# Optimization experiments

Measured on AMD Instinct MI355X. Metric: run time of the kernel, lower is better.

The kernel has to match this reference:

```python
import jax, jax.numpy as jnp
import numpy as np

B = 32768      # rows
L = 512        # sequence_length
H = 1024       # inter_layer_size
E = 128        # encoding_size
K = 8          # number of (shifting_type, transformer_ID) combinations / decoders


def setup_inputs() -> dict:
    key = jax.random.key(0)
    ks = jax.random.split(key, 8)
    feats = jax.random.normal(ks[0], (B, L), jnp.float32)
    ids = jax.random.randint(ks[1], (B,), 0, K).astype(jnp.float32)
    x = jnp.concatenate([feats, ids[:, None]], axis=1)  # [B, L+1], last col = combination ID

    def init_w(k, shape, fan_in):
        return jax.random.normal(k, shape, jnp.float32) / np.float32(np.sqrt(fan_in))

    # shared encoder: Linear(L->H), Linear(H->E)  (weights stored [in, out])
    We1 = init_w(ks[2], (L, H), L); be1 = jnp.zeros((H,), jnp.float32)
    We2 = init_w(ks[3], (H, E), H); be2 = jnp.zeros((E,), jnp.float32)
    # per-ID decoders stacked along expert dim K: Linear(E->H), Linear(H->L)
    Wd1 = init_w(ks[4], (K, E, H), E); bd1 = jnp.zeros((K, H), jnp.float32)
    Wd2 = init_w(ks[5], (K, H, L), H); bd2 = jnp.zeros((K, L), jnp.float32)
    return dict(x=x, We1=We1, be1=be1, We2=We2, be2=be2,
                Wd1=Wd1, bd1=bd1, Wd2=Wd2, bd2=bd2)


def reference(x, We1, be1, We2, be2, Wd1, bd1, Wd2, bd2):
    seq_len = We1.shape[0]
    n_experts = Wd1.shape[0]
    ids = x[:, seq_len].astype(jnp.int32)          # routing column
    # torch code emits rows grouped by unique ID (torch.unique returns sorted ids);
    # jnp.argsort is stable, so within-group original order is preserved.
    order = jnp.argsort(ids)
    xs = x[order, :seq_len]                        # [B, L] grouped features
    ids_s = ids[order]                             # [B]

    # shared encoder MLP (LeakyReLU slope 0.01, torch default)
    h = jax.nn.leaky_relu(xs @ We1 + be1)          # [B, H]
    z = jax.nn.leaky_relu(h @ We2 + be2)           # [B, E]

    # dense expert dispatch: run every decoder, select per-row expert via one-hot
    hd = jax.nn.leaky_relu(jnp.einsum('be,keh->kbh', z, Wd1) + bd1[:, None, :])  # [K, B, H]
    y_all = jnp.einsum('kbh,khl->kbl', hd, Wd2) + bd2[:, None, :]                # [K, B, L]
    onehot = (ids_s[None, :] == jnp.arange(n_experts)[:, None]).astype(y_all.dtype)  # [K, B]
    return jnp.einsum('kb,kbl->bl', onehot, y_all)  # [B, L]
```

## Files before the change

kernel.cpp:

```cpp
#include <hip/hip_runtime.h>
#include <hip/hip_bf16.h>

#define B_ROWS 32768
#define L_DIM 512
#define H_DIM 1024
#define E_DIM 128
#define K_EXP 8
#define NBLK 128
#define MAXT 264
#define MAXB (MAXT * 128)

typedef __bf16 bf16x8 __attribute__((ext_vector_type(8)));
typedef float f32x4 __attribute__((ext_vector_type(4)));

__device__ __forceinline__ void gload16(const void* src, void* dst) {
    __builtin_amdgcn_global_load_lds(
        (const __attribute__((address_space(1))) unsigned int*)src,
        (__attribute__((address_space(3))) unsigned int*)dst, 16, 0, 0);
}

#define M_NT 0
#define M_SEG 1
#define M_SEGP 10
#define M_CNT 19
#define M_TEXP 27

__global__ void k_ids_hist(const float* __restrict__ x, int* __restrict__ ids,
                           int* __restrict__ hist) {
    __shared__ int lh[K_EXP];
    int t = threadIdx.x;
    if (t < K_EXP) lh[t] = 0;
    __syncthreads();
    int i = blockIdx.x * 256 + t;
    int id = (int)x[(size_t)i * (L_DIM + 1) + L_DIM];
    ids[i] = id;
    atomicAdd(&lh[id], 1);
    __syncthreads();
    if (t < K_EXP) hist[blockIdx.x * K_EXP + t] = lh[t];
}

__global__ void k_scan(const int* __restrict__ hist, int* __restrict__ base,
                       int* __restrict__ meta, int* __restrict__ order_pad) {
    __shared__ int c[K_EXP];
    __shared__ int sp[K_EXP + 1];
    __shared__ int scnt[K_EXP];
    int k = threadIdx.x;
    if (k < K_EXP) {
        int run = 0;
        for (int b = 0; b < NBLK; ++b) {
            base[b * K_EXP + k] = run;
            run += hist[b * K_EXP + k];
        }
        c[k] = run;
    }
    __syncthreads();
    if (k == 0) {
        int s = 0, p = 0;
        for (int e = 0; e < K_EXP; ++e) {
            meta[M_SEG + e] = s;
            meta[M_SEGP + e] = p;
            meta[M_CNT + e] = c[e];
            sp[e] = p;
            scnt[e] = c[e];
            s += c[e];
            p += ((c[e] + 127) >> 7) << 7;
        }
        meta[M_SEG + K_EXP] = s;
        meta[M_SEGP + K_EXP] = p;
        sp[K_EXP] = p;
        int nT = p >> 7;
        meta[M_NT] = nT;
        for (int e = 0; e < K_EXP; ++e)
            for (int t2 = sp[e] >> 7; t2 < sp[e + 1] >> 7; ++t2)
                meta[M_TEXP + t2] = e;
        for (int t2 = nT; t2 < MAXT; ++t2) meta[M_TEXP + t2] = 0;
    }
    __syncthreads();
    if (k < K_EXP) {
        int s0 = sp[k];
        for (int b = 0; b < NBLK; ++b) base[b * K_EXP + k] += s0;
    }
    for (int e = 0; e < K_EXP; ++e) {
        int st = sp[e] + scnt[e], en = sp[e + 1];
        for (int p2 = st + k; p2 < en; p2 += 64) order_pad[p2] = 0;
    }
    for (int p2 = sp[K_EXP] + k; p2 < MAXB; p2 += 64) order_pad[p2] = 0;
}

__global__ void k_order(const int* __restrict__ ids, const int* __restrict__ base,
                        int* __restrict__ order) {
    __shared__ int sid[256];
    int t = threadIdx.x;
    int i = blockIdx.x * 256 + t;
    int my = ids[i];
    sid[t] = my;
    __syncthreads();
    int rank = 0;
    for (int j = 0; j < t; ++j) rank += (sid[j] == my) ? 1 : 0;
    order[base[blockIdx.x * K_EXP + my] + rank] = i;
}

__global__ void k_gather(const float* __restrict__ x, const int* __restrict__ order,
                         __hip_bfloat16* __restrict__ xs) {
    int idx = blockIdx.x * 256 + threadIdx.x;
    int p = idx >> 7;
    int c4 = (idx & 127) << 2;
    int src = order[p];
    const float* sp = x + (size_t)src * (L_DIM + 1) + c4;
    __hip_bfloat16 v[4];
    v[0] = __float2bfloat16(sp[0]);
    v[1] = __float2bfloat16(sp[1]);
    v[2] = __float2bfloat16(sp[2]);
    v[3] = __float2bfloat16(sp[3]);
    *(uint2*)(xs + (size_t)p * L_DIM + c4) = *(uint2*)v;
}

__global__ void k_transpose(const float* __restrict__ W, __hip_bfloat16* __restrict__ Wt,
                            int KDim, int NDim) {
    __shared__ float tile[32][33];
    int k0 = blockIdx.x << 5, n0 = blockIdx.y << 5;
    const float* Wb = W + (size_t)blockIdx.z * KDim * NDim;
    __hip_bfloat16* Wtb = Wt + (size_t)blockIdx.z * KDim * NDim;
    int tx = threadIdx.x & 31, ty = threadIdx.x >> 5;
    for (int i = ty; i < 32; i += 8)
        tile[i][tx] = Wb[(size_t)(k0 + i) * NDim + n0 + tx];
    __syncthreads();
    for (int i = ty; i < 32; i += 8)
        Wtb[(size_t)(n0 + i) * KDim + k0 + tx] = __float2bfloat16(tile[tx][i]);
}

template <int KD, int ND, bool GROUPED, bool LEAKY, bool OUT_BF16, bool MAPROW>
__launch_bounds__(256, 2)
__global__ void gemm_w(const __hip_bfloat16* __restrict__ A,
                       const __hip_bfloat16* __restrict__ Bt,
                       const float* __restrict__ bias,
                       void* __restrict__ Cout,
                       const int* __restrict__ meta) {
    constexpr int NNT = ND / 256;
    constexpr int TOT = MAXT * NNT;
    static_assert(TOT % 8 == 0, "XCD chunking needs TOT % 8 == 0");
    constexpr int ASZ = 128 * 32;
    constexpr int SLOT = ASZ + 256 * 32;
    constexpr int NK = KD / 32;

    __shared__ __align__(16) __hip_bfloat16 smem[3 * SLOT];
    const int id = blockIdx.x;
    const int wg = (id & 7) * (TOT / 8) + (id >> 3);
    const int mt = wg / NNT, nt = wg % NNT;
    const int m0 = mt << 7, n0 = nt << 8;
    const __hip_bfloat16* Bp = Bt;
    const float* bp = bias;
    int e = 0;
    if (GROUPED) {
        e = meta[M_TEXP + mt];
        Bp += (size_t)e * KD * ND;
        bp += (size_t)e * ND;
    }
    const int t = threadIdx.x, w = t >> 6, l = t & 63;
    const int g = l >> 4, li = l & 15;
    const int r0 = l >> 2, s0 = l & 3;

    f32x4 acc[8][4];
#pragma unroll
    for (int i = 0; i < 8; ++i)
#pragma unroll
        for (int j = 0; j < 4; ++j) acc[i][j] = (f32x4){0.f, 0.f, 0.f, 0.f};

    auto stage = [&](int b, int kt) {
#pragma unroll
        for (int qi = 0; qi < 2; ++qi) {
            int q = 2 * w + qi;
            int r = q * 16 + r0;
            int ksg = s0 ^ ((r >> 1) & 3);
            gload16(A + (size_t)(m0 + r) * KD + kt * 32 + ksg * 8,
                    &smem[b * SLOT + q * 512]);
        }
#pragma unroll
        for (int qi = 0; qi < 4; ++qi) {
            int q = 4 * w + qi;
            int r = q * 16 + r0;
            int ksg = s0 ^ ((r >> 1) & 3);
            gload16(Bp + (size_t)(n0 + r) * KD + kt * 32 + ksg * 8,
                    &smem[b * SLOT + ASZ + q * 512]);
        }
    };

    stage(0, 0);
    stage(1, 1);
    int b = 0;
    for (int kt = 0; kt < NK; ++kt) {
        if (kt == NK - 1)
            asm volatile("s_waitcnt vmcnt(0)\ns_barrier" ::: "memory");
        else
            asm volatile("s_waitcnt vmcnt(6)\ns_barrier" ::: "memory");
        __builtin_amdgcn_sched_barrier(0);
        if (kt + 2 < NK) stage((b + 2 >= 3) ? b - 1 : b + 2, kt + 2);
        bf16x8 af[8], bfr[4];
#pragma unroll
        for (int fm = 0; fm < 8; ++fm) {
            int rr = fm * 16 + li;
            int ss = g ^ ((rr >> 1) & 3);
            af[fm] = *(const bf16x8*)&smem[b * SLOT + rr * 32 + ss * 8];
        }
#pragma unroll
        for (int fn = 0; fn < 4; ++fn) {
            int cc = w * 64 + fn * 16 + li;
            int ss = g ^ ((cc >> 1) & 3);
            bfr[fn] = *(const bf16x8*)&smem[b * SLOT + ASZ + cc * 32 + ss * 8];
        }
        __builtin_amdgcn_s_setprio(1);
#pragma unroll
        for (int fm = 0; fm < 8; ++fm)
#pragma unroll
            for (int fn = 0; fn < 4; ++fn)
                acc[fm][fn] = __builtin_amdgcn_mfma_f32_16x16x32_bf16(
                    af[fm], bfr[fn], acc[fm][fn], 0, 0, 0);
        __builtin_amdgcn_s_setprio(0);
        b = (b + 1 >= 3) ? 0 : b + 1;
    }

    float bv[4];
#pragma unroll
    for (int fn = 0; fn < 4; ++fn) bv[fn] = bp[n0 + w * 64 + fn * 16 + li];
    int se = 0, sp2 = 0, ce = 0;
    if (MAPROW) { se = meta[M_SEG + e]; sp2 = meta[M_SEGP + e]; ce = meta[M_CNT + e]; }
#pragma unroll
    for (int fm = 0; fm < 8; ++fm)
#pragma unroll
        for (int i = 0; i < 4; ++i) {
            int rp = m0 + fm * 16 + g * 4 + i;
#pragma unroll
            for (int fn = 0; fn < 4; ++fn) {
                float v = acc[fm][fn][i] + bv[fn];
                if (LEAKY) v = v > 0.f ? v : 0.01f * v;
                int col = n0 + w * 64 + fn * 16 + li;
                if (MAPROW) {
                    int local = rp - sp2;
                    if (local < ce)
                        ((float*)Cout)[(size_t)(se + local) * ND + col] = v;
                } else if (OUT_BF16) {
                    ((__hip_bfloat16*)Cout)[(size_t)rp * ND + col] = __float2bfloat16(v);
                } else {
                    ((float*)Cout)[(size_t)rp * ND + col] = v;
                }
            }
        }
}

template <int KD, int ND, bool LEAKY>
__launch_bounds__(256)
__global__ void gemm_u64(const __hip_bfloat16* __restrict__ A,
                         const __hip_bfloat16* __restrict__ Bt,
                         const float* __restrict__ bias,
                         __hip_bfloat16* __restrict__ Cout) {
    constexpr int BM = 64;
    constexpr int NNT = ND / 128;
    constexpr int NMT = MAXB / BM;
    constexpr int TOT = NMT * NNT;
    static_assert(TOT % 8 == 0, "XCD chunking needs TOT % 8 == 0");
    constexpr int ACH = BM * 32;
    constexpr int SLOT = ACH + 128 * 32;
    constexpr int NK = KD / 32;

    __shared__ __align__(16) __hip_bfloat16 smem[3 * SLOT];
    const int id = blockIdx.x;
    const int wg = (id & 7) * (TOT / 8) + (id >> 3);
    const int mt = wg / NNT, nt = wg % NNT;
    const int n0 = nt << 7;
    const int m0 = mt * BM;
    const int t = threadIdx.x, w = t >> 6, l = t & 63;
    const int wm = w >> 1, wn = w & 1, g = l >> 4, li = l & 15;
    const int r0 = l >> 2, s0 = l & 3;

    f32x4 acc[2][4];
#pragma unroll
    for (int i = 0; i < 2; ++i)
#pragma unroll
        for (int j = 0; j < 4; ++j) acc[i][j] = (f32x4){0.f, 0.f, 0.f, 0.f};

    auto stage = [&](int b, int kt) {
        {
            int q = w, r = q * 16 + r0;
            int ksg = s0 ^ ((r >> 1) & 3);
            gload16(A + (size_t)(m0 + r) * KD + kt * 32 + ksg * 8,
                    &smem[b * SLOT + q * 512]);
        }
#pragma unroll
        for (int qi = 0; qi < 2; ++qi) {
            int q = 2 * w + qi, r = q * 16 + r0;
            int ksg = s0 ^ ((r >> 1) & 3);
            gload16(Bt + (size_t)(n0 + r) * KD + kt * 32 + ksg * 8,
                    &smem[b * SLOT + ACH + q * 512]);
        }
    };

    stage(0, 0);
    stage(1, 1);
    int b = 0;
    for (int kt = 0; kt < NK; ++kt) {
        if (kt == NK - 1)
            asm volatile("s_waitcnt vmcnt(0)\ns_barrier" ::: "memory");
        else
            asm volatile("s_waitcnt vmcnt(3)\ns_barrier" ::: "memory");
        __builtin_amdgcn_sched_barrier(0);
        if (kt + 2 < NK) stage((b + 2 >= 3) ? b - 1 : b + 2, kt + 2);
        bf16x8 af[2], bfr[4];
#pragma unroll
        for (int fm = 0; fm < 2; ++fm) {
            int rr = wm * 32 + fm * 16 + li;
            int ss = g ^ ((rr >> 1) & 3);
            af[fm] = *(const bf16x8*)&smem[b * SLOT + rr * 32 + ss * 8];
        }
#pragma unroll
        for (int fn = 0; fn < 4; ++fn) {
            int cc = wn * 64 + fn * 16 + li;
            int ss = g ^ ((cc >> 1) & 3);
            bfr[fn] = *(const bf16x8*)&smem[b * SLOT + ACH + cc * 32 + ss * 8];
        }
        __builtin_amdgcn_s_setprio(1);
#pragma unroll
        for (int fm = 0; fm < 2; ++fm)
#pragma unroll
            for (int fn = 0; fn < 4; ++fn)
                acc[fm][fn] = __builtin_amdgcn_mfma_f32_16x16x32_bf16(
                    af[fm], bfr[fn], acc[fm][fn], 0, 0, 0);
        __builtin_amdgcn_s_setprio(0);
        b = (b + 1 >= 3) ? 0 : b + 1;
    }

    float bv[4];
#pragma unroll
    for (int fn = 0; fn < 4; ++fn) bv[fn] = bias[n0 + wn * 64 + fn * 16 + li];
#pragma unroll
    for (int fm = 0; fm < 2; ++fm)
#pragma unroll
        for (int i = 0; i < 4; ++i) {
            int r = m0 + wm * 32 + fm * 16 + g * 4 + i;
#pragma unroll
            for (int fn = 0; fn < 4; ++fn) {
                float v = acc[fm][fn][i] + bv[fn];
                if (LEAKY) v = v > 0.f ? v : 0.01f * v;
                Cout[(size_t)r * ND + n0 + wn * 64 + fn * 16 + li] = __float2bfloat16(v);
            }
        }
}

extern "C" void kernel_launch(void* const* d_in, const int* in_sizes, int n_in,
                              void* d_out, int out_size, void* d_ws, size_t ws_size,
                              hipStream_t stream) {
    (void)in_sizes; (void)n_in; (void)out_size; (void)ws_size;
    const float* x   = (const float*)d_in[0];
    const float* We1 = (const float*)d_in[1];
    const float* be1 = (const float*)d_in[2];
    const float* We2 = (const float*)d_in[3];
    const float* be2 = (const float*)d_in[4];
    const float* Wd1 = (const float*)d_in[5];
    const float* bd1 = (const float*)d_in[6];
    const float* Wd2 = (const float*)d_in[7];
    const float* bd2 = (const float*)d_in[8];
    float* out = (float*)d_out;

    char* w = (char*)d_ws;
    auto alloc = [&](size_t bytes) {
        char* p = w;
        w += (bytes + 255) & ~(size_t)255;
        return p;
    };
    int* ids       = (int*)alloc((size_t)B_ROWS * 4);
    int* order_pad = (int*)alloc((size_t)MAXB * 4);
    int* hist      = (int*)alloc((size_t)NBLK * K_EXP * 4);
    int* base      = (int*)alloc((size_t)NBLK * K_EXP * 4);
    int* meta      = (int*)alloc((size_t)(M_TEXP + MAXT) * 4);
    __hip_bfloat16* xs   = (__hip_bfloat16*)alloc((size_t)MAXB * L_DIM * 2);
    __hip_bfloat16* hbuf = (__hip_bfloat16*)alloc((size_t)MAXB * H_DIM * 2);
    __hip_bfloat16* zbuf = (__hip_bfloat16*)alloc((size_t)MAXB * E_DIM * 2);
    __hip_bfloat16* Wt1  = (__hip_bfloat16*)alloc((size_t)L_DIM * H_DIM * 2);
    __hip_bfloat16* Wt2  = (__hip_bfloat16*)alloc((size_t)H_DIM * E_DIM * 2);
    __hip_bfloat16* Wd1t = (__hip_bfloat16*)alloc((size_t)K_EXP * E_DIM * H_DIM * 2);
    __hip_bfloat16* Wd2t = (__hip_bfloat16*)alloc((size_t)K_EXP * H_DIM * L_DIM * 2);

    k_ids_hist<<<NBLK, 256, 0, stream>>>(x, ids, hist);
    k_scan<<<1, 64, 0, stream>>>(hist, base, meta, order_pad);
    k_order<<<NBLK, 256, 0, stream>>>(ids, base, order_pad);
    k_gather<<<(MAXB * (L_DIM / 4)) / 256, 256, 0, stream>>>(x, order_pad, xs);

    k_transpose<<<dim3(L_DIM / 32, H_DIM / 32, 1), 256, 0, stream>>>(We1, Wt1, L_DIM, H_DIM);
    k_transpose<<<dim3(H_DIM / 32, E_DIM / 32, 1), 256, 0, stream>>>(We2, Wt2, H_DIM, E_DIM);
    k_transpose<<<dim3(E_DIM / 32, H_DIM / 32, K_EXP), 256, 0, stream>>>(Wd1, Wd1t, E_DIM, H_DIM);
    k_transpose<<<dim3(H_DIM / 32, L_DIM / 32, K_EXP), 256, 0, stream>>>(Wd2, Wd2t, H_DIM, L_DIM);

    gemm_w<L_DIM, H_DIM, false, true, true, false>
        <<<MAXT * (H_DIM / 256), 256, 0, stream>>>(xs, Wt1, be1, hbuf, meta);
    gemm_u64<H_DIM, E_DIM, true>
        <<<(MAXB / 64) * (E_DIM / 128), 256, 0, stream>>>(hbuf, Wt2, be2, zbuf);
    gemm_w<E_DIM, H_DIM, true, true, true, false>
        <<<MAXT * (H_DIM / 256), 256, 0, stream>>>(zbuf, Wd1t, bd1, hbuf, meta);
    gemm_w<H_DIM, L_DIM, true, false, false, true>
        <<<MAXT * (L_DIM / 256), 256, 0, stream>>>(hbuf, Wd2t, bd2, out, meta);
}
```

Before: 229.8 us.

## Use 256x256 eight-wave GEMM tiles with 64-wide K ping-pong and regroup padding

Expert segments are now padded to 256 rows, and the large GEMMs (encoder layer 1 and decoder layer 2) use a new 512-thread kernel with 256x256 tiles. It double-buffers 64-wide K tiles with an XOR swizzle and interleaves LDS reads, MFMA bursts and half-tile async stages behind barriers. Decoder layer 1 (K=128) gets a dedicated 128x128 kernel that looks up its expert per 256-row group. The goal is more data reuse per LDS byte and better overlap of loads with MFMA, at the cost of more padding rows, more barriers and heavier register pressure.

```diff
diff --git a/kernel.cpp b/kernel.cpp
--- a/kernel.cpp
+++ b/kernel.cpp
@@ -7,8 +7,8 @@
 #define E_DIM 128
 #define K_EXP 8
 #define NBLK 128
-#define MAXT 264
-#define MAXB (MAXT * 128)
+#define MAXT2 136
+#define MAXB2 (MAXT2 * 256)
 
 typedef __bf16 bf16x8 __attribute__((ext_vector_type(8)));
 typedef float f32x4 __attribute__((ext_vector_type(4)));
@@ -63,17 +63,17 @@
             sp[e] = p;
             scnt[e] = c[e];
             s += c[e];
-            p += ((c[e] + 127) >> 7) << 7;
+            p += ((c[e] + 255) >> 8) << 8;
         }
         meta[M_SEG + K_EXP] = s;
         meta[M_SEGP + K_EXP] = p;
         sp[K_EXP] = p;
-        int nT = p >> 7;
+        int nT = p >> 8;
         meta[M_NT] = nT;
         for (int e = 0; e < K_EXP; ++e)
-            for (int t2 = sp[e] >> 7; t2 < sp[e + 1] >> 7; ++t2)
+            for (int t2 = sp[e] >> 8; t2 < (sp[e + 1] >> 8); ++t2)
                 meta[M_TEXP + t2] = e;
-        for (int t2 = nT; t2 < MAXT; ++t2) meta[M_TEXP + t2] = 0;
+        for (int t2 = nT; t2 < MAXT2; ++t2) meta[M_TEXP + t2] = 0;
     }
     __syncthreads();
     if (k < K_EXP) {
@@ -84,7 +84,7 @@
         int st = sp[e] + scnt[e], en = sp[e + 1];
         for (int p2 = st + k; p2 < en; p2 += 64) order_pad[p2] = 0;
     }
-    for (int p2 = sp[K_EXP] + k; p2 < MAXB; p2 += 64) order_pad[p2] = 0;
+    for (int p2 = sp[K_EXP] + k; p2 < MAXB2; p2 += 64) order_pad[p2] = 0;
 }
 
 __global__ void k_order(const int* __restrict__ ids, const int* __restrict__ base,
@@ -129,25 +129,32 @@
         Wtb[(size_t)(n0 + i) * KDim + k0 + tx] = __float2bfloat16(tile[tx][i]);
 }
 
+#define BARRIER asm volatile("s_barrier" ::: "memory")
+#define LGKM0   asm volatile("s_waitcnt lgkmcnt(0)" ::: "memory")
+#define VM4BAR  asm volatile("s_waitcnt vmcnt(4)\ns_barrier" ::: "memory")
+#define VM0BAR  asm volatile("s_waitcnt vmcnt(0)\ns_barrier" ::: "memory")
+
 template <int KD, int ND, bool GROUPED, bool LEAKY, bool OUT_BF16, bool MAPROW>
-__launch_bounds__(256, 2)
-__global__ void gemm_w(const __hip_bfloat16* __restrict__ A,
-                       const __hip_bfloat16* __restrict__ Bt,
-                       const float* __restrict__ bias,
-                       void* __restrict__ Cout,
-                       const int* __restrict__ meta) {
+__launch_bounds__(512, 2)
+__global__ void gemm8(const __hip_bfloat16* __restrict__ A,
+                      const __hip_bfloat16* __restrict__ Bt,
+                      const float* __restrict__ bias,
+                      void* __restrict__ Cout,
+                      const int* __restrict__ meta) {
     constexpr int NNT = ND / 256;
-    constexpr int TOT = MAXT * NNT;
-    static_assert(TOT % 8 == 0, "XCD chunking needs TOT % 8 == 0");
-    constexpr int ASZ = 128 * 32;
-    constexpr int SLOT = ASZ + 256 * 32;
-    constexpr int NK = KD / 32;
-
-    __shared__ __align__(16) __hip_bfloat16 smem[3 * SLOT];
+    constexpr int TOT = MAXT2 * NNT;
+    static_assert(TOT % 8 == 0, "XCD chunking");
+    constexpr int NKT = KD / 64;
+    constexpr int NI = NKT / 2;
+    static_assert(NKT % 2 == 0, "even K-tiles");
+    constexpr int DBUF = 32768;
+
+    __shared__ __align__(16) __hip_bfloat16 smem[2 * DBUF];
+
     const int id = blockIdx.x;
     const int wg = (id & 7) * (TOT / 8) + (id >> 3);
     const int mt = wg / NNT, nt = wg % NNT;
-    const int m0 = mt << 7, n0 = nt << 8;
+    const int m0 = mt << 8, n0 = nt << 8;
     const __hip_bfloat16* Bp = Bt;
     const float* bp = bias;
     int e = 0;
@@ -156,9 +163,11 @@
         Bp += (size_t)e * KD * ND;
         bp += (size_t)e * ND;
     }
-    const int t = threadIdx.x, w = t >> 6, l = t & 63;
+    const int t = threadIdx.x;
+    const int w = t >> 6, l = t & 63;
+    const int wm = w >> 2, wn = w & 3;
     const int g = l >> 4, li = l & 15;
-    const int r0 = l >> 2, s0 = l & 3;
+    const int sr = l >> 3, sc = l & 7;
 
     f32x4 acc[8][4];
 #pragma unroll
@@ -166,74 +175,89 @@
 #pragma unroll
         for (int j = 0; j < 4; ++j) acc[i][j] = (f32x4){0.f, 0.f, 0.f, 0.f};
 
-    auto stage = [&](int b, int kt) {
-#pragma unroll
-        for (int qi = 0; qi < 2; ++qi) {
-            int q = 2 * w + qi;
-            int r = q * 16 + r0;
-            int ksg = s0 ^ ((r >> 1) & 3);
-            gload16(A + (size_t)(m0 + r) * KD + kt * 32 + ksg * 8,
-                    &smem[b * SLOT + q * 512]);
-        }
-#pragma unroll
-        for (int qi = 0; qi < 4; ++qi) {
-            int q = 4 * w + qi;
-            int r = q * 16 + r0;
-            int ksg = s0 ^ ((r >> 1) & 3);
-            gload16(Bp + (size_t)(n0 + r) * KD + kt * 32 + ksg * 8,
-                    &smem[b * SLOT + ASZ + q * 512]);
-        }
-    };
-
-    stage(0, 0);
-    stage(1, 1);
-    int b = 0;
-    for (int kt = 0; kt < NK; ++kt) {
-        if (kt == NK - 1)
-            asm volatile("s_waitcnt vmcnt(0)\ns_barrier" ::: "memory");
-        else
-            asm volatile("s_waitcnt vmcnt(6)\ns_barrier" ::: "memory");
+    auto stageH = [&](int d, int which, int half, int kt) {
+        const __hip_bfloat16* src = which ? Bp : A;
+        const int rb = (which ? n0 : m0) + half * 128;
+#pragma unroll
+        for (int q = 0; q < 2; ++q) {
+            int rl = (q * 8 + w) * 8;
+            gload16(src + (size_t)(rb + rl + sr) * KD + (size_t)(kt * 8 + (sc ^ sr)) * 8,
+                    &smem[d * DBUF + which * 16384 + half * 8192 + rl * 64]);
+        }
+    };
+
+    bf16x8 a0[8], a1[8], bb[2];
+    auto LDA = [&](int d, int ksub, bf16x8* ar) {
+#pragma unroll
+        for (int fm = 0; fm < 8; ++fm) {
+            int r = wm * 128 + fm * 16 + li;
+            ar[fm] = *(const bf16x8*)&smem[d * DBUF + r * 64 + (((ksub << 2) + g) ^ (r & 7)) * 8];
+        }
+    };
+    auto LDB = [&](int d, int np, int ksub) {
+#pragma unroll
+        for (int j = 0; j < 2; ++j) {
+            int r = wn * 64 + (np * 2 + j) * 16 + li;
+            bb[j] = *(const bf16x8*)&smem[d * DBUF + 16384 + r * 64 + (((ksub << 2) + g) ^ (r & 7)) * 8];
+        }
+    };
+    auto MM = [&](int np, bf16x8* ar) {
+        __builtin_amdgcn_s_setprio(1);
+#pragma unroll
+        for (int fm = 0; fm < 8; ++fm) {
+            acc[fm][np * 2 + 0] = __builtin_amdgcn_mfma_f32_16x16x32_bf16(
+                ar[fm], bb[0], acc[fm][np * 2 + 0], 0, 0, 0);
+            acc[fm][np * 2 + 1] = __builtin_amdgcn_mfma_f32_16x16x32_bf16(
+                ar[fm], bb[1], acc[fm][np * 2 + 1], 0, 0, 0);
+        }
+        __builtin_amdgcn_s_setprio(0);
+    };
+
+    stageH(0, 0, 0, 0); stageH(0, 0, 1, 0);
+    stageH(0, 1, 0, 0); stageH(0, 1, 1, 0);
+    stageH(1, 0, 0, 1); stageH(1, 0, 1, 1);
+    VM4BAR;
+    __builtin_amdgcn_sched_barrier(0);
+
+    for (int i = 0; i < NI; ++i) {
+        const int E2 = 2 * i + 2, O1 = 2 * i + 1, O2 = 2 * i + 3;
+        const bool more = (i + 1 < NI);
+        LDA(0, 0, a0); LDB(0, 0, 0); stageH(1, 1, 0, O1);
+        BARRIER; LGKM0; MM(0, a0); BARRIER;
+        LDA(0, 1, a1); LDB(0, 0, 1); stageH(1, 1, 1, O1);
+        BARRIER; LGKM0; MM(0, a1); BARRIER;
+        LDB(0, 1, 0); if (more) stageH(0, 0, 0, E2);
+        BARRIER; LGKM0; MM(1, a0); BARRIER;
+        LDB(0, 1, 1); if (more) stageH(0, 0, 1, E2);
+        BARRIER; LGKM0; MM(1, a1);
+        if (more) { VM4BAR; } else { VM0BAR; }
         __builtin_amdgcn_sched_barrier(0);
-        if (kt + 2 < NK) stage((b + 2 >= 3) ? b - 1 : b + 2, kt + 2);
-        bf16x8 af[8], bfr[4];
-#pragma unroll
-        for (int fm = 0; fm < 8; ++fm) {
-            int rr = fm * 16 + li;
-            int ss = g ^ ((rr >> 1) & 3);
-            af[fm] = *(const bf16x8*)&smem[b * SLOT + rr * 32 + ss * 8];
-        }
-#pragma unroll
-        for (int fn = 0; fn < 4; ++fn) {
-            int cc = w * 64 + fn * 16 + li;
-            int ss = g ^ ((cc >> 1) & 3);
-            bfr[fn] = *(const bf16x8*)&smem[b * SLOT + ASZ + cc * 32 + ss * 8];
-        }
-        __builtin_amdgcn_s_setprio(1);
-#pragma unroll
-        for (int fm = 0; fm < 8; ++fm)
-#pragma unroll
-            for (int fn = 0; fn < 4; ++fn)
-                acc[fm][fn] = __builtin_amdgcn_mfma_f32_16x16x32_bf16(
-                    af[fm], bfr[fn], acc[fm][fn], 0, 0, 0);
-        __builtin_amdgcn_s_setprio(0);
-        b = (b + 1 >= 3) ? 0 : b + 1;
+        LDA(1, 0, a0); LDB(1, 0, 0); if (more) stageH(0, 1, 0, E2);
+        BARRIER; LGKM0; MM(0, a0); BARRIER;
+        LDA(1, 1, a1); LDB(1, 0, 1); if (more) stageH(0, 1, 1, E2);
+        BARRIER; LGKM0; MM(0, a1); BARRIER;
+        LDB(1, 1, 0); if (more) stageH(1, 0, 0, O2);
+        BARRIER; LGKM0; MM(1, a0); BARRIER;
+        LDB(1, 1, 1); if (more) stageH(1, 0, 1, O2);
+        BARRIER; LGKM0; MM(1, a1);
+        if (more) { VM4BAR; __builtin_amdgcn_sched_barrier(0); }
     }
 
     float bv[4];
 #pragma unroll
-    for (int fn = 0; fn < 4; ++fn) bv[fn] = bp[n0 + w * 64 + fn * 16 + li];
+    for (int fn = 0; fn < 4; ++fn) bv[fn] = bp[n0 + wn * 64 + fn * 16 + li];
     int se = 0, sp2 = 0, ce = 0;
     if (MAPROW) { se = meta[M_SEG + e]; sp2 = meta[M_SEGP + e]; ce = meta[M_CNT + e]; }
 #pragma unroll
     for (int fm = 0; fm < 8; ++fm)
 #pragma unroll
-        for (int i = 0; i < 4; ++i) {
-            int rp = m0 + fm * 16 + g * 4 + i;
+        for (int ii = 0; ii < 4; ++ii) {
+            int rp = m0 + wm * 128 + fm * 16 + g * 4 + ii;
 #pragma unroll
             for (int fn = 0; fn < 4; ++fn) {
-                float v = acc[fm][fn][i] + bv[fn];
+                float v = acc[fm][fn][ii] + bv[fn];
                 if (LEAKY) v = v > 0.f ? v : 0.01f * v;
-                int col = n0 + w * 64 + fn * 16 + li;
+                int col = n0 + wn * 64 + fn * 16 + li;
                 if (MAPROW) {
                     int local = rp - sp2;
                     if (local < ce)
@@ -247,6 +271,102 @@
         }
 }
 
+template <int ND, bool LEAKY>
+__launch_bounds__(256)
+__global__ void gemm_g3(const __hip_bfloat16* __restrict__ A,
+                        const __hip_bfloat16* __restrict__ Bt,
+                        const float* __restrict__ bias,
+                        __hip_bfloat16* __restrict__ Cout,
+                        const int* __restrict__ meta) {
+    constexpr int KD = 128;
+    constexpr int NNT = ND / 128;
+    constexpr int TOT = (MAXB2 / 128) * NNT;
+    static_assert(TOT % 8 == 0, "XCD chunking");
+    constexpr int SLOT = 2 * 128 * 32;
+    constexpr int NK = KD / 32;
+    __shared__ __align__(16) __hip_bfloat16 smem[3 * SLOT];
+    const int id = blockIdx.x;
+    const int wg = (id & 7) * (TOT / 8) + (id >> 3);
+    const int mt = wg / NNT, nt = wg % NNT;
+    const int e = meta[M_TEXP + (mt >> 1)];
+    const int m0 = mt << 7, n0 = nt << 7;
+    const __hip_bfloat16* Bp = Bt + (size_t)e * KD * ND;
+    const float* bp = bias + (size_t)e * ND;
+    const int t = threadIdx.x, w = t >> 6, l = t & 63;
+    const int wm = w >> 1, wn = w & 1, g = l >> 4, li = l & 15;
+    const int q0 = 2 * w, r0 = l >> 2, s0 = l & 3;
+
+    f32x4 acc[4][4];
+#pragma unroll
+    for (int i = 0; i < 4; ++i)
+#pragma unroll
+        for (int j = 0; j < 4; ++j) acc[i][j] = (f32x4){0.f, 0.f, 0.f, 0.f};
+
+    auto stage = [&](int b, int kt) {
+#pragma unroll
+        for (int qi = 0; qi < 2; ++qi) {
+            int q = q0 + qi, r = q * 16 + r0;
+            int ksg = s0 ^ ((r >> 1) & 3);
+            gload16(A + (size_t)(m0 + r) * KD + kt * 32 + ksg * 8,
+                    &smem[b * SLOT + q * 512]);
+        }
+#pragma unroll
+        for (int qi = 0; qi < 2; ++qi) {
+            int q = q0 + qi, r = q * 16 + r0;
+            int ksg = s0 ^ ((r >> 1) & 3);
+            gload16(Bp + (size_t)(n0 + r) * KD + kt * 32 + ksg * 8,
+                    &smem[b * SLOT + 4096 + q * 512]);
+        }
+    };
+
+    stage(0, 0);
+    stage(1, 1);
+    int b = 0;
+    for (int kt = 0; kt < NK; ++kt) {
+        if (kt == NK - 1) { VM0BAR; } else { VM4BAR; }
+        __builtin_amdgcn_sched_barrier(0);
+        if (kt + 2 < NK) stage((b + 2 >= 3) ? b - 1 : b + 2, kt + 2);
+        bf16x8 af[4], bfr[4];
+#pragma unroll
+        for (int fm = 0; fm < 4; ++fm) {
+            int rr = wm * 64 + fm * 16 + li;
+            int ss = g ^ ((rr >> 1) & 3);
+            af[fm] = *(const bf16x8*)&smem[b * SLOT + rr * 32 + ss * 8];
+        }
+#pragma unroll
+        for (int fn = 0; fn < 4; ++fn) {
+            int cc = wn * 64 + fn * 16 + li;
+            int ss = g ^ ((cc >> 1) & 3);
+            bfr[fn] = *(const bf16x8*)&smem[b * SLOT + 4096 + cc * 32 + ss * 8];
+        }
+        __builtin_amdgcn_s_setprio(1);
+#pragma unroll
+        for (int fm = 0; fm < 4; ++fm)
+#pragma unroll
+            for (int fn = 0; fn < 4; ++fn)
+                acc[fm][fn] = __builtin_amdgcn_mfma_f32_16x16x32_bf16(
+                    af[fm], bfr[fn], acc[fm][fn], 0, 0, 0);
+        __builtin_amdgcn_s_setprio(0);
+        b = (b + 1 >= 3) ? 0 : b + 1;
+    }
+
+    float bv[4];
+#pragma unroll
+    for (int fn = 0; fn < 4; ++fn) bv[fn] = bp[n0 + wn * 64 + fn * 16 + li];
+#pragma unroll
+    for (int fm = 0; fm < 4; ++fm)
+#pragma unroll
+        for (int i = 0; i < 4; ++i) {
+            int r = m0 + wm * 64 + fm * 16 + g * 4 + i;
+#pragma unroll
+            for (int fn = 0; fn < 4; ++fn) {
+                float v = acc[fm][fn][i] + bv[fn];
+                if (LEAKY) v = v > 0.f ? v : 0.01f * v;
+                Cout[(size_t)r * ND + n0 + wn * 64 + fn * 16 + li] = __float2bfloat16(v);
+            }
+        }
+}
+
 template <int KD, int ND, bool LEAKY>
 __launch_bounds__(256)
 __global__ void gemm_u64(const __hip_bfloat16* __restrict__ A,
@@ -255,9 +375,9 @@
                          __hip_bfloat16* __restrict__ Cout) {
     constexpr int BM = 64;
     constexpr int NNT = ND / 128;
-    constexpr int NMT = MAXB / BM;
+    constexpr int NMT = MAXB2 / BM;
     constexpr int TOT = NMT * NNT;
-    static_assert(TOT % 8 == 0, "XCD chunking needs TOT % 8 == 0");
+    static_assert(TOT % 8 == 0, "XCD chunking");
     constexpr int ACH = BM * 32;
     constexpr int SLOT = ACH + 128 * 32;
     constexpr int NK = KD / 32;
@@ -367,13 +487,13 @@
         return p;
     };
     int* ids       = (int*)alloc((size_t)B_ROWS * 4);
-    int* order_pad = (int*)alloc((size_t)MAXB * 4);
+    int* order_pad = (int*)alloc((size_t)MAXB2 * 4);
     int* hist      = (int*)alloc((size_t)NBLK * K_EXP * 4);
     int* base      = (int*)alloc((size_t)NBLK * K_EXP * 4);
-    int* meta      = (int*)alloc((size_t)(M_TEXP + MAXT) * 4);
-    __hip_bfloat16* xs   = (__hip_bfloat16*)alloc((size_t)MAXB * L_DIM * 2);
-    __hip_bfloat16* hbuf = (__hip_bfloat16*)alloc((size_t)MAXB * H_DIM * 2);
-    __hip_bfloat16* zbuf = (__hip_bfloat16*)alloc((size_t)MAXB * E_DIM * 2);
+    int* meta      = (int*)alloc((size_t)(M_TEXP + MAXT2) * 4);
+    __hip_bfloat16* xs   = (__hip_bfloat16*)alloc((size_t)MAXB2 * L_DIM * 2);
+    __hip_bfloat16* hbuf = (__hip_bfloat16*)alloc((size_t)MAXB2 * H_DIM * 2);
+    __hip_bfloat16* zbuf = (__hip_bfloat16*)alloc((size_t)MAXB2 * E_DIM * 2);
     __hip_bfloat16* Wt1  = (__hip_bfloat16*)alloc((size_t)L_DIM * H_DIM * 2);
     __hip_bfloat16* Wt2  = (__hip_bfloat16*)alloc((size_t)H_DIM * E_DIM * 2);
     __hip_bfloat16* Wd1t = (__hip_bfloat16*)alloc((size_t)K_EXP * E_DIM * H_DIM * 2);
@@ -382,19 +502,19 @@
     k_ids_hist<<<NBLK, 256, 0, stream>>>(x, ids, hist);
     k_scan<<<1, 64, 0, stream>>>(hist, base, meta, order_pad);
     k_order<<<NBLK, 256, 0, stream>>>(ids, base, order_pad);
-    k_gather<<<(MAXB * (L_DIM / 4)) / 256, 256, 0, stream>>>(x, order_pad, xs);
+    k_gather<<<(MAXB2 * (L_DIM / 4)) / 256, 256, 0, stream>>>(x, order_pad, xs);
 
     k_transpose<<<dim3(L_DIM / 32, H_DIM / 32, 1), 256, 0, stream>>>(We1, Wt1, L_DIM, H_DIM);
     k_transpose<<<dim3(H_DIM / 32, E_DIM / 32, 1), 256, 0, stream>>>(We2, Wt2, H_DIM, E_DIM);
     k_transpose<<<dim3(E_DIM / 32, H_DIM / 32, K_EXP), 256, 0, stream>>>(Wd1, Wd1t, E_DIM, H_DIM);
     k_transpose<<<dim3(H_DIM / 32, L_DIM / 32, K_EXP), 256, 0, stream>>>(Wd2, Wd2t, H_DIM, L_DIM);
 
-    gemm_w<L_DIM, H_DIM, false, true, true, false>
-        <<<MAXT * (H_DIM / 256), 256, 0, stream>>>(xs, Wt1, be1, hbuf, meta);
+    gemm8<L_DIM, H_DIM, false, true, true, false>
+        <<<MAXT2 * (H_DIM / 256), 512, 0, stream>>>(xs, Wt1, be1, hbuf, meta);
     gemm_u64<H_DIM, E_DIM, true>
-        <<<(MAXB / 64) * (E_DIM / 128), 256, 0, stream>>>(hbuf, Wt2, be2, zbuf);
-    gemm_w<E_DIM, H_DIM, true, true, true, false>
-        <<<MAXT * (H_DIM / 256), 256, 0, stream>>>(zbuf, Wd1t, bd1, hbuf, meta);
-    gemm_w<H_DIM, L_DIM, true, false, false, true>
-        <<<MAXT * (L_DIM / 256), 256, 0, stream>>>(hbuf, Wd2t, bd2, out, meta);
-}
+        <<<(MAXB2 / 64) * (E_DIM / 128), 256, 0, stream>>>(hbuf, Wt2, be2, zbuf);
+    gemm_g3<H_DIM, true>
+        <<<(MAXB2 / 128) * (H_DIM / 128), 256, 0, stream>>>(zbuf, Wd1t, bd1, hbuf, meta);
+    gemm8<H_DIM, L_DIM, true, false, false, true>
+        <<<MAXT2 * (L_DIM / 256), 512, 0, stream>>>(hbuf, Wd2t, bd2, out, meta);
+}
```

New measurement: 286.0 us. +24.4%, slower.

## Fuse encoder-out and decoder-in GEMMs via LDS, merge transposes, retile GEMMs

Applied to the files above, without the earlier changes.

The second encoder GEMM (H->E) and the first decoder GEMM (E->H) now run in one kernel per 64-row tile. The latent z stays in swizzled LDS instead of making a round trip through a global buffer. The four weight-transpose launches become one kernel that dispatches on block index. The first and last GEMMs move from 128x256 tiles with 8x4 fragments per wave to 128x128 tiles with a 2x2 wave grid. This trades more blocks and less register pressure for more reloading of the A tiles. The fused kernel writes its output over the hidden buffer it reads, which relies on each block reading only its own rows.

```diff
diff --git a/kernel.cpp b/kernel.cpp
--- a/kernel.cpp
+++ b/kernel.cpp
@@ -115,73 +115,80 @@
     *(uint2*)(xs + (size_t)p * L_DIM + c4) = *(uint2*)v;
 }
 
-__global__ void k_transpose(const float* __restrict__ W, __hip_bfloat16* __restrict__ Wt,
-                            int KDim, int NDim) {
+__global__ void k_wtrans(const float* __restrict__ We1, const float* __restrict__ We2,
+                         const float* __restrict__ Wd1, const float* __restrict__ Wd2,
+                         __hip_bfloat16* __restrict__ Wt1, __hip_bfloat16* __restrict__ Wt2,
+                         __hip_bfloat16* __restrict__ Wd1t, __hip_bfloat16* __restrict__ Wd2t) {
     __shared__ float tile[32][33];
-    int k0 = blockIdx.x << 5, n0 = blockIdx.y << 5;
-    const float* Wb = W + (size_t)blockIdx.z * KDim * NDim;
-    __hip_bfloat16* Wtb = Wt + (size_t)blockIdx.z * KDim * NDim;
+    int b = blockIdx.x;
+    const float* W;
+    __hip_bfloat16* Wt;
+    int KDim, NDim, local;
+    if (b < 512)       { W = We1; Wt = Wt1; KDim = 512;  NDim = 1024; local = b; }
+    else if (b < 640)  { W = We2; Wt = Wt2; KDim = 1024; NDim = 128;  local = b - 512; }
+    else if (b < 1664) {
+        int lb = b - 640;
+        int e = lb >> 7;
+        local = lb & 127;
+        KDim = 128; NDim = 1024;
+        W = Wd1 + (size_t)e * KDim * NDim;
+        Wt = Wd1t + (size_t)e * KDim * NDim;
+    } else {
+        int lb = b - 1664;
+        int e = lb >> 9;
+        local = lb & 511;
+        KDim = 1024; NDim = 512;
+        W = Wd2 + (size_t)e * KDim * NDim;
+        Wt = Wd2t + (size_t)e * KDim * NDim;
+    }
+    int ntK = KDim >> 5;
+    int k0 = (local % ntK) << 5, n0 = (local / ntK) << 5;
     int tx = threadIdx.x & 31, ty = threadIdx.x >> 5;
     for (int i = ty; i < 32; i += 8)
-        tile[i][tx] = Wb[(size_t)(k0 + i) * NDim + n0 + tx];
+        tile[i][tx] = W[(size_t)(k0 + i) * NDim + n0 + tx];
     __syncthreads();
     for (int i = ty; i < 32; i += 8)
-        Wtb[(size_t)(n0 + i) * KDim + k0 + tx] = __float2bfloat16(tile[tx][i]);
-}
-
-template <int KD, int ND, bool GROUPED, bool LEAKY, bool OUT_BF16, bool MAPROW>
-__launch_bounds__(256, 2)
-__global__ void gemm_w(const __hip_bfloat16* __restrict__ A,
-                       const __hip_bfloat16* __restrict__ Bt,
-                       const float* __restrict__ bias,
-                       void* __restrict__ Cout,
-                       const int* __restrict__ meta) {
-    constexpr int NNT = ND / 256;
+        Wt[(size_t)(n0 + i) * KDim + k0 + tx] = __float2bfloat16(tile[tx][i]);
+}
+
+__global__ __launch_bounds__(256) void gemm_g1(const __hip_bfloat16* __restrict__ A,
+                                               const __hip_bfloat16* __restrict__ Bt,
+                                               const float* __restrict__ bias,
+                                               __hip_bfloat16* __restrict__ Cout) {
+    constexpr int KD = L_DIM, ND = H_DIM;
+    constexpr int NNT = ND / 128;
     constexpr int TOT = MAXT * NNT;
-    static_assert(TOT % 8 == 0, "XCD chunking needs TOT % 8 == 0");
-    constexpr int ASZ = 128 * 32;
-    constexpr int SLOT = ASZ + 256 * 32;
+    constexpr int SLOT = 2 * 128 * 32;
     constexpr int NK = KD / 32;
-
     __shared__ __align__(16) __hip_bfloat16 smem[3 * SLOT];
     const int id = blockIdx.x;
     const int wg = (id & 7) * (TOT / 8) + (id >> 3);
     const int mt = wg / NNT, nt = wg % NNT;
-    const int m0 = mt << 7, n0 = nt << 8;
-    const __hip_bfloat16* Bp = Bt;
-    const float* bp = bias;
-    int e = 0;
-    if (GROUPED) {
-        e = meta[M_TEXP + mt];
-        Bp += (size_t)e * KD * ND;
-        bp += (size_t)e * ND;
-    }
+    const int m0 = mt << 7, n0 = nt << 7;
     const int t = threadIdx.x, w = t >> 6, l = t & 63;
-    const int g = l >> 4, li = l & 15;
-    const int r0 = l >> 2, s0 = l & 3;
-
-    f32x4 acc[8][4];
-#pragma unroll
-    for (int i = 0; i < 8; ++i)
+    const int wm = w >> 1, wn = w & 1, g = l >> 4, li = l & 15;
+    const int q0 = 2 * w, r0 = l >> 2, s0 = l & 3;
+
+    f32x4 acc[4][4];
+#pragma unroll
+    for (int i = 0; i < 4; ++i)
 #pragma unroll
         for (int j = 0; j < 4; ++j) acc[i][j] = (f32x4){0.f, 0.f, 0.f, 0.f};
 
     auto stage = [&](int b, int kt) {
 #pragma unroll
         for (int qi = 0; qi < 2; ++qi) {
-            int q = 2 * w + qi;
-            int r = q * 16 + r0;
+            int q = q0 + qi, r = q * 16 + r0;
             int ksg = s0 ^ ((r >> 1) & 3);
             gload16(A + (size_t)(m0 + r) * KD + kt * 32 + ksg * 8,
                     &smem[b * SLOT + q * 512]);
         }
 #pragma unroll
-        for (int qi = 0; qi < 4; ++qi) {
-            int q = 4 * w + qi;
-            int r = q * 16 + r0;
-            int ksg = s0 ^ ((r >> 1) & 3);
-            gload16(Bp + (size_t)(n0 + r) * KD + kt * 32 + ksg * 8,
-                    &smem[b * SLOT + ASZ + q * 512]);
+        for (int qi = 0; qi < 2; ++qi) {
+            int q = q0 + qi, r = q * 16 + r0;
+            int ksg = s0 ^ ((r >> 1) & 3);
+            gload16(Bt + (size_t)(n0 + r) * KD + kt * 32 + ksg * 8,
+                    &smem[b * SLOT + 4096 + q * 512]);
         }
     };
 
@@ -192,25 +199,25 @@
         if (kt == NK - 1)
             asm volatile("s_waitcnt vmcnt(0)\ns_barrier" ::: "memory");
         else
-            asm volatile("s_waitcnt vmcnt(6)\ns_barrier" ::: "memory");
+            asm volatile("s_waitcnt vmcnt(4)\ns_barrier" ::: "memory");
         __builtin_amdgcn_sched_barrier(0);
         if (kt + 2 < NK) stage((b + 2 >= 3) ? b - 1 : b + 2, kt + 2);
-        bf16x8 af[8], bfr[4];
-#pragma unroll
-        for (int fm = 0; fm < 8; ++fm) {
-            int rr = fm * 16 + li;
+        bf16x8 af[4], bfr[4];
+#pragma unroll
+        for (int fm = 0; fm < 4; ++fm) {
+            int rr = wm * 64 + fm * 16 + li;
             int ss = g ^ ((rr >> 1) & 3);
             af[fm] = *(const bf16x8*)&smem[b * SLOT + rr * 32 + ss * 8];
         }
 #pragma unroll
         for (int fn = 0; fn < 4; ++fn) {
-            int cc = w * 64 + fn * 16 + li;
+            int cc = wn * 64 + fn * 16 + li;
             int ss = g ^ ((cc >> 1) & 3);
-            bfr[fn] = *(const bf16x8*)&smem[b * SLOT + ASZ + cc * 32 + ss * 8];
+            bfr[fn] = *(const bf16x8*)&smem[b * SLOT + 4096 + cc * 32 + ss * 8];
         }
         __builtin_amdgcn_s_setprio(1);
 #pragma unroll
-        for (int fm = 0; fm < 8; ++fm)
+        for (int fm = 0; fm < 4; ++fm)
 #pragma unroll
             for (int fn = 0; fn < 4; ++fn)
                 acc[fm][fn] = __builtin_amdgcn_mfma_f32_16x16x32_bf16(
@@ -221,76 +228,230 @@
 
     float bv[4];
 #pragma unroll
-    for (int fn = 0; fn < 4; ++fn) bv[fn] = bp[n0 + w * 64 + fn * 16 + li];
-    int se = 0, sp2 = 0, ce = 0;
-    if (MAPROW) { se = meta[M_SEG + e]; sp2 = meta[M_SEGP + e]; ce = meta[M_CNT + e]; }
-#pragma unroll
-    for (int fm = 0; fm < 8; ++fm)
+    for (int fn = 0; fn < 4; ++fn) bv[fn] = bias[n0 + wn * 64 + fn * 16 + li];
+#pragma unroll
+    for (int fm = 0; fm < 4; ++fm)
 #pragma unroll
         for (int i = 0; i < 4; ++i) {
-            int rp = m0 + fm * 16 + g * 4 + i;
+            int r = m0 + wm * 64 + fm * 16 + g * 4 + i;
 #pragma unroll
             for (int fn = 0; fn < 4; ++fn) {
                 float v = acc[fm][fn][i] + bv[fn];
-                if (LEAKY) v = v > 0.f ? v : 0.01f * v;
-                int col = n0 + w * 64 + fn * 16 + li;
-                if (MAPROW) {
-                    int local = rp - sp2;
-                    if (local < ce)
-                        ((float*)Cout)[(size_t)(se + local) * ND + col] = v;
-                } else if (OUT_BF16) {
-                    ((__hip_bfloat16*)Cout)[(size_t)rp * ND + col] = __float2bfloat16(v);
-                } else {
-                    ((float*)Cout)[(size_t)rp * ND + col] = v;
+                v = v > 0.f ? v : 0.01f * v;
+                Cout[(size_t)r * ND + n0 + wn * 64 + fn * 16 + li] = __float2bfloat16(v);
+            }
+        }
+}
+
+__global__ __launch_bounds__(256) void gemm_g23(const __hip_bfloat16* __restrict__ h,
+                                                const __hip_bfloat16* __restrict__ Wt2,
+                                                const float* __restrict__ be2,
+                                                const __hip_bfloat16* __restrict__ Wd1t,
+                                                const float* __restrict__ bd1,
+                                                __hip_bfloat16* __restrict__ hd,
+                                                const int* __restrict__ meta) {
+    constexpr int SLOTA = 64 * 32 + 128 * 32;
+    constexpr int SLOTB = 128 * 32;
+    constexpr int NKA = H_DIM / 32;
+    __shared__ __align__(16) __hip_bfloat16 smem[3 * SLOTA + 64 * 128];
+    __hip_bfloat16* zl = smem + 3 * SLOTA;
+
+    const int id = blockIdx.x;
+    const int wg = (id & 7) * 66 + (id >> 3);
+    const int m0 = wg << 6;
+    const int e = meta[M_TEXP + (wg >> 1)];
+    const int t = threadIdx.x, w = t >> 6, l = t & 63;
+    const int wm = w >> 1, wn = w & 1, g = l >> 4, li = l & 15;
+    const int r0 = l >> 2, s0 = l & 3;
+
+    f32x4 accA[2][4];
+#pragma unroll
+    for (int i = 0; i < 2; ++i)
+#pragma unroll
+        for (int j = 0; j < 4; ++j) accA[i][j] = (f32x4){0.f, 0.f, 0.f, 0.f};
+
+    auto stageA = [&](int b, int kt) {
+        {
+            int q = w, r = q * 16 + r0;
+            int ksg = s0 ^ ((r >> 1) & 3);
+            gload16(h + (size_t)(m0 + r) * H_DIM + kt * 32 + ksg * 8,
+                    &smem[b * SLOTA + q * 512]);
+        }
+#pragma unroll
+        for (int qi = 0; qi < 2; ++qi) {
+            int q = 2 * w + qi, r = q * 16 + r0;
+            int ksg = s0 ^ ((r >> 1) & 3);
+            gload16(Wt2 + (size_t)r * H_DIM + kt * 32 + ksg * 8,
+                    &smem[b * SLOTA + 2048 + q * 512]);
+        }
+    };
+
+    stageA(0, 0);
+    stageA(1, 1);
+    int b = 0;
+    for (int kt = 0; kt < NKA; ++kt) {
+        if (kt == NKA - 1)
+            asm volatile("s_waitcnt vmcnt(0)\ns_barrier" ::: "memory");
+        else
+            asm volatile("s_waitcnt vmcnt(3)\ns_barrier" ::: "memory");
+        __builtin_amdgcn_sched_barrier(0);
+        if (kt + 2 < NKA) stageA((b + 2 >= 3) ? b - 1 : b + 2, kt + 2);
+        bf16x8 af[2], bfr[4];
+#pragma unroll
+        for (int fm = 0; fm < 2; ++fm) {
+            int rr = wm * 32 + fm * 16 + li;
+            int ss = g ^ ((rr >> 1) & 3);
+            af[fm] = *(const bf16x8*)&smem[b * SLOTA + rr * 32 + ss * 8];
+        }
+#pragma unroll
+        for (int fn = 0; fn < 4; ++fn) {
+            int cc = wn * 64 + fn * 16 + li;
+            int ss = g ^ ((cc >> 1) & 3);
+            bfr[fn] = *(const bf16x8*)&smem[b * SLOTA + 2048 + cc * 32 + ss * 8];
+        }
+        __builtin_amdgcn_s_setprio(1);
+#pragma unroll
+        for (int fm = 0; fm < 2; ++fm)
+#pragma unroll
+            for (int fn = 0; fn < 4; ++fn)
+                accA[fm][fn] = __builtin_amdgcn_mfma_f32_16x16x32_bf16(
+                    af[fm], bfr[fn], accA[fm][fn], 0, 0, 0);
+        __builtin_amdgcn_s_setprio(0);
+        b = (b + 1 >= 3) ? 0 : b + 1;
+    }
+
+#pragma unroll
+    for (int fm = 0; fm < 2; ++fm)
+#pragma unroll
+        for (int i = 0; i < 4; ++i) {
+            int r = wm * 32 + fm * 16 + g * 4 + i;
+            int swr = (r >> 1) & 3;
+#pragma unroll
+            for (int fn = 0; fn < 4; ++fn) {
+                int c = wn * 64 + fn * 16 + li;
+                float v = accA[fm][fn][i] + be2[c];
+                v = v > 0.f ? v : 0.01f * v;
+                int kt = c >> 5, k32 = c & 31;
+                zl[kt * 2048 + r * 32 + (((k32 >> 3) ^ swr) << 3) + (k32 & 7)] =
+                    __float2bfloat16(v);
+            }
+        }
+    __syncthreads();
+
+    const __hip_bfloat16* Bp = Wd1t + (size_t)e * H_DIM * E_DIM;
+    const float* bp = bd1 + (size_t)e * H_DIM;
+
+    auto stageB = [&](int bb, int step) {
+        int chunk = step >> 2, kt = step & 3;
+#pragma unroll
+        for (int qi = 0; qi < 2; ++qi) {
+            int q = 2 * w + qi, r = q * 16 + r0;
+            int ksg = s0 ^ ((r >> 1) & 3);
+            gload16(Bp + (size_t)(chunk * 128 + r) * E_DIM + kt * 32 + ksg * 8,
+                    &smem[bb * SLOTB + q * 512]);
+        }
+    };
+
+    f32x4 accB[2][4];
+#pragma unroll
+    for (int i = 0; i < 2; ++i)
+#pragma unroll
+        for (int j = 0; j < 4; ++j) accB[i][j] = (f32x4){0.f, 0.f, 0.f, 0.f};
+
+    stageB(0, 0);
+    stageB(1, 1);
+    b = 0;
+    for (int step = 0; step < 32; ++step) {
+        int chunk = step >> 2, kt = step & 3;
+        if (step == 31)
+            asm volatile("s_waitcnt vmcnt(0)\ns_barrier" ::: "memory");
+        else
+            asm volatile("s_waitcnt vmcnt(2)\ns_barrier" ::: "memory");
+        __builtin_amdgcn_sched_barrier(0);
+        if (step + 2 < 32) stageB((b + 2 >= 3) ? b - 1 : b + 2, step + 2);
+        bf16x8 af[2], bfr[4];
+#pragma unroll
+        for (int fm = 0; fm < 2; ++fm) {
+            int rr = wm * 32 + fm * 16 + li;
+            int ss = g ^ ((rr >> 1) & 3);
+            af[fm] = *(const bf16x8*)&zl[kt * 2048 + rr * 32 + ss * 8];
+        }
+#pragma unroll
+        for (int fn = 0; fn < 4; ++fn) {
+            int cc = wn * 64 + fn * 16 + li;
+            int ss = g ^ ((cc >> 1) & 3);
+            bfr[fn] = *(const bf16x8*)&smem[b * SLOTB + cc * 32 + ss * 8];
+        }
+        __builtin_amdgcn_s_setprio(1);
+#pragma unroll
+        for (int fm = 0; fm < 2; ++fm)
+#pragma unroll
+            for (int fn = 0; fn < 4; ++fn)
+                accB[fm][fn] = __builtin_amdgcn_mfma_f32_16x16x32_bf16(
+                    af[fm], bfr[fn], accB[fm][fn], 0, 0, 0);
+        __builtin_amdgcn_s_setprio(0);
+        if (kt == 3) {
+#pragma unroll
+            for (int fm = 0; fm < 2; ++fm)
+#pragma unroll
+                for (int i = 0; i < 4; ++i) {
+                    int r = m0 + wm * 32 + fm * 16 + g * 4 + i;
+#pragma unroll
+                    for (int fn = 0; fn < 4; ++fn) {
+                        int c = chunk * 128 + wn * 64 + fn * 16 + li;
+                        float v = accB[fm][fn][i] + bp[c];
+                        v = v > 0.f ? v : 0.01f * v;
+                        hd[(size_t)r * H_DIM + c] = __float2bfloat16(v);
+                        accB[fm][fn][i] = 0.f;
+                    }
                 }
-            }
-        }
-}
-
-template <int KD, int ND, bool LEAKY>
-__launch_bounds__(256)
-__global__ void gemm_u64(const __hip_bfloat16* __restrict__ A,
-                         const __hip_bfloat16* __restrict__ Bt,
-                         const float* __restrict__ bias,
-                         __hip_bfloat16* __restrict__ Cout) {
-    constexpr int BM = 64;
+        }
+        b = (b + 1 >= 3) ? 0 : b + 1;
+    }
+}
+
+__global__ __launch_bounds__(256) void gemm_g4(const __hip_bfloat16* __restrict__ A,
+                                               const __hip_bfloat16* __restrict__ Bt,
+                                               const float* __restrict__ bias,
+                                               float* __restrict__ Cout,
+                                               const int* __restrict__ meta) {
+    constexpr int KD = H_DIM, ND = L_DIM;
     constexpr int NNT = ND / 128;
-    constexpr int NMT = MAXB / BM;
-    constexpr int TOT = NMT * NNT;
-    static_assert(TOT % 8 == 0, "XCD chunking needs TOT % 8 == 0");
-    constexpr int ACH = BM * 32;
-    constexpr int SLOT = ACH + 128 * 32;
+    constexpr int TOT = MAXT * NNT;
+    constexpr int SLOT = 2 * 128 * 32;
     constexpr int NK = KD / 32;
-
     __shared__ __align__(16) __hip_bfloat16 smem[3 * SLOT];
     const int id = blockIdx.x;
     const int wg = (id & 7) * (TOT / 8) + (id >> 3);
     const int mt = wg / NNT, nt = wg % NNT;
-    const int n0 = nt << 7;
-    const int m0 = mt * BM;
+    const int e = meta[M_TEXP + mt];
+    const int m0 = mt << 7, n0 = nt << 7;
+    const __hip_bfloat16* Bp = Bt + (size_t)e * KD * ND;
+    const float* bp = bias + (size_t)e * ND;
     const int t = threadIdx.x, w = t >> 6, l = t & 63;
     const int wm = w >> 1, wn = w & 1, g = l >> 4, li = l & 15;
-    const int r0 = l >> 2, s0 = l & 3;
-
-    f32x4 acc[2][4];
-#pragma unroll
-    for (int i = 0; i < 2; ++i)
+    const int q0 = 2 * w, r0 = l >> 2, s0 = l & 3;
+
+    f32x4 acc[4][4];
+#pragma unroll
+    for (int i = 0; i < 4; ++i)
 #pragma unroll
         for (int j = 0; j < 4; ++j) acc[i][j] = (f32x4){0.f, 0.f, 0.f, 0.f};
 
     auto stage = [&](int b, int kt) {
-        {
-            int q = w, r = q * 16 + r0;
+#pragma unroll
+        for (int qi = 0; qi < 2; ++qi) {
+            int q = q0 + qi, r = q * 16 + r0;
             int ksg = s0 ^ ((r >> 1) & 3);
             gload16(A + (size_t)(m0 + r) * KD + kt * 32 + ksg * 8,
                     &smem[b * SLOT + q * 512]);
         }
 #pragma unroll
         for (int qi = 0; qi < 2; ++qi) {
-            int q = 2 * w + qi, r = q * 16 + r0;
-            int ksg = s0 ^ ((r >> 1) & 3);
-            gload16(Bt + (size_t)(n0 + r) * KD + kt * 32 + ksg * 8,
-                    &smem[b * SLOT + ACH + q * 512]);
+            int q = q0 + qi, r = q * 16 + r0;
+            int ksg = s0 ^ ((r >> 1) & 3);
+            gload16(Bp + (size_t)(n0 + r) * KD + kt * 32 + ksg * 8,
+                    &smem[b * SLOT + 4096 + q * 512]);
         }
     };
 
@@ -301,13 +462,13 @@
         if (kt == NK - 1)
             asm volatile("s_waitcnt vmcnt(0)\ns_barrier" ::: "memory");
         else
-            asm volatile("s_waitcnt vmcnt(3)\ns_barrier" ::: "memory");
+            asm volatile("s_waitcnt vmcnt(4)\ns_barrier" ::: "memory");
         __builtin_amdgcn_sched_barrier(0);
         if (kt + 2 < NK) stage((b + 2 >= 3) ? b - 1 : b + 2, kt + 2);
-        bf16x8 af[2], bfr[4];
-#pragma unroll
-        for (int fm = 0; fm < 2; ++fm) {
-            int rr = wm * 32 + fm * 16 + li;
+        bf16x8 af[4], bfr[4];
+#pragma unroll
+        for (int fm = 0; fm < 4; ++fm) {
+            int rr = wm * 64 + fm * 16 + li;
             int ss = g ^ ((rr >> 1) & 3);
             af[fm] = *(const bf16x8*)&smem[b * SLOT + rr * 32 + ss * 8];
         }
@@ -315,11 +476,11 @@
         for (int fn = 0; fn < 4; ++fn) {
             int cc = wn * 64 + fn * 16 + li;
             int ss = g ^ ((cc >> 1) & 3);
-            bfr[fn] = *(const bf16x8*)&smem[b * SLOT + ACH + cc * 32 + ss * 8];
+            bfr[fn] = *(const bf16x8*)&smem[b * SLOT + 4096 + cc * 32 + ss * 8];
         }
         __builtin_amdgcn_s_setprio(1);
 #pragma unroll
-        for (int fm = 0; fm < 2; ++fm)
+        for (int fm = 0; fm < 4; ++fm)
 #pragma unroll
             for (int fn = 0; fn < 4; ++fn)
                 acc[fm][fn] = __builtin_amdgcn_mfma_f32_16x16x32_bf16(
@@ -330,17 +491,20 @@
 
     float bv[4];
 #pragma unroll
-    for (int fn = 0; fn < 4; ++fn) bv[fn] = bias[n0 + wn * 64 + fn * 16 + li];
-#pragma unroll
-    for (int fm = 0; fm < 2; ++fm)
+    for (int fn = 0; fn < 4; ++fn) bv[fn] = bp[n0 + wn * 64 + fn * 16 + li];
+    const int se = meta[M_SEG + e], sp2 = meta[M_SEGP + e], ce = meta[M_CNT + e];
+#pragma unroll
+    for (int fm = 0; fm < 4; ++fm)
 #pragma unroll
         for (int i = 0; i < 4; ++i) {
-            int r = m0 + wm * 32 + fm * 16 + g * 4 + i;
-#pragma unroll
-            for (int fn = 0; fn < 4; ++fn) {
-                float v = acc[fm][fn][i] + bv[fn];
-                if (LEAKY) v = v > 0.f ? v : 0.01f * v;
-                Cout[(size_t)r * ND + n0 + wn * 64 + fn * 16 + li] = __float2bfloat16(v);
+            int rp = m0 + wm * 64 + fm * 16 + g * 4 + i;
+            int local = rp - sp2;
+            if (local < ce) {
+#pragma unroll
+                for (int fn = 0; fn < 4; ++fn) {
+                    float v = acc[fm][fn][i] + bv[fn];
+                    Cout[(size_t)(se + local) * ND + n0 + wn * 64 + fn * 16 + li] = v;
+                }
             }
         }
 }
@@ -373,7 +537,6 @@
     int* meta      = (int*)alloc((size_t)(M_TEXP + MAXT) * 4);
     __hip_bfloat16* xs   = (__hip_bfloat16*)alloc((size_t)MAXB * L_DIM * 2);
     __hip_bfloat16* hbuf = (__hip_bfloat16*)alloc((size_t)MAXB * H_DIM * 2);
-    __hip_bfloat16* zbuf = (__hip_bfloat16*)alloc((size_t)MAXB * E_DIM * 2);
     __hip_bfloat16* Wt1  = (__hip_bfloat16*)alloc((size_t)L_DIM * H_DIM * 2);
     __hip_bfloat16* Wt2  = (__hip_bfloat16*)alloc((size_t)H_DIM * E_DIM * 2);
     __hip_bfloat16* Wd1t = (__hip_bfloat16*)alloc((size_t)K_EXP * E_DIM * H_DIM * 2);
@@ -383,18 +546,9 @@
     k_scan<<<1, 64, 0, stream>>>(hist, base, meta, order_pad);
     k_order<<<NBLK, 256, 0, stream>>>(ids, base, order_pad);
     k_gather<<<(MAXB * (L_DIM / 4)) / 256, 256, 0, stream>>>(x, order_pad, xs);
-
-    k_transpose<<<dim3(L_DIM / 32, H_DIM / 32, 1), 256, 0, stream>>>(We1, Wt1, L_DIM, H_DIM);
-    k_transpose<<<dim3(H_DIM / 32, E_DIM / 32, 1), 256, 0, stream>>>(We2, Wt2, H_DIM, E_DIM);
-    k_transpose<<<dim3(E_DIM / 32, H_DIM / 32, K_EXP), 256, 0, stream>>>(Wd1, Wd1t, E_DIM, H_DIM);
-    k_transpose<<<dim3(H_DIM / 32, L_DIM / 32, K_EXP), 256, 0, stream>>>(Wd2, Wd2t, H_DIM, L_DIM);
-
-    gemm_w<L_DIM, H_DIM, false, true, true, false>
-        <<<MAXT * (H_DIM / 256), 256, 0, stream>>>(xs, Wt1, be1, hbuf, meta);
-    gemm_u64<H_DIM, E_DIM, true>
-        <<<(MAXB / 64) * (E_DIM / 128), 256, 0, stream>>>(hbuf, Wt2, be2, zbuf);
-    gemm_w<E_DIM, H_DIM, true, true, true, false>
-        <<<MAXT * (H_DIM / 256), 256, 0, stream>>>(zbuf, Wd1t, bd1, hbuf, meta);
-    gemm_w<H_DIM, L_DIM, true, false, false, true>
-        <<<MAXT * (L_DIM / 256), 256, 0, stream>>>(hbuf, Wd2t, bd2, out, meta);
-}
+    k_wtrans<<<5760, 256, 0, stream>>>(We1, We2, Wd1, Wd2, Wt1, Wt2, Wd1t, Wd2t);
+
+    gemm_g1<<<MAXT * (H_DIM / 128), 256, 0, stream>>>(xs, Wt1, be1, hbuf);
+    gemm_g23<<<MAXB / 64, 256, 0, stream>>>(hbuf, Wt2, be2, Wd1t, bd1, hbuf, meta);
+    gemm_g4<<<MAXT * (L_DIM / 128), 256, 0, stream>>>(hbuf, Wd2t, bd2, out, meta);
+}
```

Result: faster. 208.3 us (-9.4%).
